# Performance work log

Measured on AMD Instinct MI355X. Metric: run time of the kernel, lower is better.

Reference implementation:

```python
import jax, jax.numpy as jnp
import numpy as np

B, S, D, H, E, K = 2, 2048, 1024, 2048, 8, 2


def setup_inputs() -> dict:
    key = jax.random.key(0)
    ks = jax.random.split(key, 9)
    sc_d = 1.0 / np.sqrt(D)
    sc_h = 1.0 / np.sqrt(H)
    return {
        "x": jax.random.normal(ks[0], (B, S, D), dtype=jnp.float32),
        "w_router": jax.random.normal(ks[1], (E, D), dtype=jnp.float32) * sc_d,
        "Wg": jax.random.normal(ks[2], (E, H, D), dtype=jnp.float32) * sc_d,  # per-expert gate proj (torch Linear weight layout [out,in])
        "Wu": jax.random.normal(ks[3], (E, H, D), dtype=jnp.float32) * sc_d,
        "Wd": jax.random.normal(ks[4], (E, D, H), dtype=jnp.float32) * sc_h,
        "sg": jax.random.normal(ks[5], (H, D), dtype=jnp.float32) * sc_d,  # shared expert
        "su": jax.random.normal(ks[6], (H, D), dtype=jnp.float32) * sc_d,
        "sd": jax.random.normal(ks[7], (D, H), dtype=jnp.float32) * sc_h,
    }


def reference(x, w_router, Wg, Wu, Wd, sg, su, sd):
    b, s, d = x.shape
    xf = x.reshape(-1, d)  # [T, D]

    # --- gating ---
    logits = jnp.einsum("td,ed->te", xf, w_router)
    probs = jax.nn.softmax(logits, axis=-1)  # [T, E]
    topw, topi = jax.lax.top_k(probs, K)  # [T, K]
    topw = topw / jnp.sum(topw, axis=-1, keepdims=True)
    # combine weights per (token, expert): topk indices are distinct per token
    comb = jnp.sum(topw[..., None] * jax.nn.one_hot(topi, E, dtype=xf.dtype), axis=1)  # [T, E]

    # --- shared expert (SwiGLU) ---
    shared = jnp.einsum(
        "th,dh->td",
        jax.nn.silu(jnp.einsum("td,hd->th", xf, sg)) * jnp.einsum("td,hd->th", xf, su),
        sd,
    )

    # --- routed experts: dense all-expert compute, weighted combine ---
    h1 = jax.nn.silu(jnp.einsum("td,ehd->teh", xf, Wg))
    h2 = jnp.einsum("td,ehd->teh", xf, Wu)
    eo = jnp.einsum("teh,edh->ted", h1 * h2, Wd)  # [T, E, D]
    routed = jnp.einsum("te,ted->td", comb, eo)

    return (routed + shared).reshape(b, s, d)
```

## Files before the change

### kernel.cpp

```cpp
#include <hip/hip_runtime.h>
#include <hip/hip_bf16.h>

#define T_TOK 4096
#define D_DIM 1024
#define H_DIM 2048

typedef __attribute__((ext_vector_type(8))) short short8;
typedef __attribute__((ext_vector_type(4))) float floatx4;

__device__ __forceinline__ unsigned short f2bf(float f) {
  unsigned int u = __builtin_bit_cast(unsigned int, f);
  return (unsigned short)((u + 0x7fffu + ((u >> 16) & 1u)) >> 16);
}

__device__ __forceinline__ float bf2f(unsigned short s) {
  unsigned int u = ((unsigned int)s) << 16;
  return __builtin_bit_cast(float, u);
}

__device__ __forceinline__ void glds16(const ushort* g, ushort* l) {
  __builtin_amdgcn_global_load_lds(
      (const __attribute__((address_space(1))) unsigned int*)g,
      (__attribute__((address_space(3))) unsigned int*)l, 16, 0, 0);
}

__global__ void cvt_kernel(const float4* __restrict__ Wg, ushort4* __restrict__ Wgb,
                           const float4* __restrict__ Wu, ushort4* __restrict__ Wub,
                           const float4* __restrict__ sg, ushort4* __restrict__ sgb,
                           const float4* __restrict__ su, ushort4* __restrict__ sub) {
  int id = blockIdx.x * 256 + threadIdx.x;
  const float4* s; ushort4* d; int i;
  if (id < 4194304)      { s = Wg; d = Wgb; i = id; }
  else if (id < 8388608) { s = Wu; d = Wub; i = id - 4194304; }
  else if (id < 8912896) { s = sg; d = sgb; i = id - 8388608; }
  else                   { s = su; d = sub; i = id - 8912896; }
  float4 v = s[i];
  ushort4 o;
  o.x = f2bf(v.x); o.y = f2bf(v.y); o.z = f2bf(v.z); o.w = f2bf(v.w);
  d[i] = o;
}

__global__ void router_kernel(const float* __restrict__ x, const float* __restrict__ wr,
                              ushort* __restrict__ xb,
                              int* __restrict__ topi, float2* __restrict__ topw) {
  const int w = threadIdx.x >> 6;
  const int l = threadIdx.x & 63;
  const int t = blockIdx.x * 4 + w;
  const float4* xr = (const float4*)(x + (size_t)t * D_DIM);
  ushort4* xo = (ushort4*)(xb + (size_t)t * D_DIM);
  float p[8];
#pragma unroll
  for (int e = 0; e < 8; ++e) p[e] = 0.f;
#pragma unroll
  for (int i = 0; i < 4; ++i) {
    float4 xv = xr[i * 64 + l];
    ushort4 o;
    o.x = f2bf(xv.x); o.y = f2bf(xv.y); o.z = f2bf(xv.z); o.w = f2bf(xv.w);
    xo[i * 64 + l] = o;
#pragma unroll
    for (int e = 0; e < 8; ++e) {
      float4 wv = ((const float4*)(wr + e * D_DIM))[i * 64 + l];
      p[e] += xv.x * wv.x + xv.y * wv.y + xv.z * wv.z + xv.w * wv.w;
    }
  }
#pragma unroll
  for (int off = 32; off > 0; off >>= 1) {
#pragma unroll
    for (int e = 0; e < 8; ++e) p[e] += __shfl_xor(p[e], off, 64);
  }
  if (l == 0) {
    float mx = p[0];
#pragma unroll
    for (int e = 1; e < 8; ++e) mx = fmaxf(mx, p[e]);
    float pr[8];
#pragma unroll
    for (int e = 0; e < 8; ++e) pr[e] = __expf(p[e] - mx);
    int i0 = 0;
#pragma unroll
    for (int e = 1; e < 8; ++e) if (pr[e] > pr[i0]) i0 = e;
    int i1 = (i0 == 0) ? 1 : 0;
#pragma unroll
    for (int e = 0; e < 8; ++e) if (e != i0 && pr[e] > pr[i1]) i1 = e;
    float w0 = pr[i0], w1 = pr[i1];
    float inv = 1.f / (w0 + w1);
    topi[t] = i0 | (i1 << 8);
    topw[t] = make_float2(w0 * inv, w1 * inv);
  }
}

__global__ void build_lists_kernel(const int* __restrict__ topi,
                                   int* __restrict__ counts, int* __restrict__ list,
                                   int* __restrict__ pos) {
  const int e = blockIdx.x;
  const int tid = threadIdx.x;
  const int l = tid & 63;
  const int w = tid >> 6;
  __shared__ int wtot[4];
  int base = 0;
  for (int c = 0; c < T_TOK; c += 256) {
    int t = c + tid;
    int ti = topi[t];
    int e0 = ti & 255, e1 = ti >> 8;
    bool flag = (e0 == e) || (e1 == e);
    unsigned long long m = __ballot(flag);
    int lanepos = __popcll(m & ((1ull << l) - 1ull));
    if (l == 0) wtot[w] = __popcll(m);
    __syncthreads();
    int waveoff = 0;
#pragma unroll
    for (int i = 0; i < 4; ++i) waveoff += (i < w) ? wtot[i] : 0;
    int tot = wtot[0] + wtot[1] + wtot[2] + wtot[3];
    if (flag) {
      int p = base + waveoff + lanepos;
      list[e * T_TOK + p] = t;
      int slot = (e0 == e) ? 0 : 1;
      pos[t * 2 + slot] = p;
    }
    base += tot;
    __syncthreads();
  }
  if (tid == 0) counts[e] = base;
}

__global__ __launch_bounds__(256, 2)
void gemm1_kernel(const ushort* __restrict__ xb,
                  const ushort* __restrict__ Wgb, const ushort* __restrict__ Wub,
                  const ushort* __restrict__ sgb, const ushort* __restrict__ sub,
                  const float4* __restrict__ Wd, ushort4* __restrict__ Wdb,
                  const float4* __restrict__ sd, ushort4* __restrict__ sdb,
                  const int* __restrict__ list, const int* __restrict__ counts,
                  ushort* __restrict__ h) {
  const int tid = threadIdx.x;
  {
    int bid = blockIdx.x + 16 * blockIdx.y + 512 * blockIdx.z;
#pragma unroll
    for (int it = 0; it < 4; ++it) {
      int idx = (bid * 4 + it) * 256 + tid;
      if (idx < 4194304) {
        float4 v = Wd[idx];
        ushort4 o;
        o.x = f2bf(v.x); o.y = f2bf(v.y); o.z = f2bf(v.z); o.w = f2bf(v.w);
        Wdb[idx] = o;
      }
    }
    if (bid < 2048) {
      int idx = bid * 256 + tid;
      float4 v = sd[idx];
      ushort4 o;
      o.x = f2bf(v.x); o.y = f2bf(v.y); o.z = f2bf(v.z); o.w = f2bf(v.w);
      sdb[idx] = o;
    }
  }

  const int e = blockIdx.z;
  int n_e, hbase;
  {
    int acc = 0, ce = 0;
    for (int q = 0; q < 8; ++q) {
      int c = counts[q];
      if (q < e) acc += c;
      if (q == e) ce = c;
    }
    n_e = (e == 8) ? T_TOK : ce;
    hbase = (e == 8) ? 8192 : acc;
  }
  const int r0 = blockIdx.y * 128;
  if (r0 >= n_e) return;
  const int c0 = blockIdx.x * 128;
  const ushort* Wg = (e == 8) ? sgb : (Wgb + (size_t)e * H_DIM * D_DIM);
  const ushort* Wu = (e == 8) ? sub : (Wub + (size_t)e * H_DIM * D_DIM);
  const int hrow0 = hbase + r0;

  __shared__ __align__(16) ushort As[128 * 64];
  __shared__ __align__(16) ushort Bgs[128 * 64];
  __shared__ __align__(16) ushort Bus[128 * 64];
  __shared__ int toks[128];

  const int l = tid & 63;
  const int w = tid >> 6;

  if (tid < 128) {
    int rr = r0 + tid;
    toks[tid] = (e == 8) ? ((rr < T_TOK) ? rr : (T_TOK - 1))
                         : list[e * T_TOK + ((rr < n_e) ? rr : (n_e - 1))];
  }
  __syncthreads();

  const int lrow8 = l >> 3;
  const int csw = (((l & 7) ^ lrow8) << 3);
  const ushort* ap[4];
#pragma unroll
  for (int i = 0; i < 4; ++i) {
    int ri = (w * 4 + i) * 8 + lrow8;
    ap[i] = xb + (size_t)toks[ri] * D_DIM + csw;
  }
  const ushort* bgp = Wg + (size_t)(c0 + w * 32 + lrow8) * D_DIM + csw;
  const ushort* bup = Wu + (size_t)(c0 + w * 32 + lrow8) * D_DIM + csw;

  floatx4 accg[4][4], accu[4][4];
#pragma unroll
  for (int i = 0; i < 4; ++i)
#pragma unroll
    for (int j = 0; j < 4; ++j) {
      accg[i][j] = (floatx4)(0.f);
      accu[i][j] = (floatx4)(0.f);
    }

  const int mrow = (w & 1) * 64;
  const int ncol = (w >> 1) * 64;
  int rba[4], rbb[4];
#pragma unroll
  for (int i = 0; i < 4; ++i) {
    rba[i] = (mrow + 16 * i + (l & 15)) * 64;
    rbb[i] = (ncol + 16 * i + (l & 15)) * 64;
  }

  for (int k0 = 0; k0 < D_DIM; k0 += 64) {
    __syncthreads();
#pragma unroll
    for (int i = 0; i < 4; ++i) {
      glds16(ap[i] + k0,                As  + (w * 4 + i) * 512);
      glds16(bgp + k0 + i * 8 * D_DIM,  Bgs + (w * 4 + i) * 512);
      glds16(bup + k0 + i * 8 * D_DIM,  Bus + (w * 4 + i) * 512);
    }
    __syncthreads();
#pragma unroll
    for (int s = 0; s < 2; ++s) {
      const int pq = ((((s << 2) | (l >> 4)) ^ (l & 7)) << 3);
      short8 a[4], bg[4], bu[4];
#pragma unroll
      for (int i = 0; i < 4; ++i) a[i] = *(const short8*)(As + rba[i] + pq);
#pragma unroll
      for (int j = 0; j < 4; ++j) {
        bg[j] = *(const short8*)(Bgs + rbb[j] + pq);
        bu[j] = *(const short8*)(Bus + rbb[j] + pq);
      }
#pragma unroll
      for (int i = 0; i < 4; ++i)
#pragma unroll
        for (int j = 0; j < 4; ++j) {
          accg[i][j] = __builtin_amdgcn_mfma_f32_16x16x32_bf16(a[i], bg[j], accg[i][j], 0, 0, 0);
          accu[i][j] = __builtin_amdgcn_mfma_f32_16x16x32_bf16(a[i], bu[j], accu[i][j], 0, 0, 0);
        }
    }
  }

#pragma unroll
  for (int i = 0; i < 4; ++i) {
#pragma unroll
    for (int r = 0; r < 4; ++r) {
      int lrow = mrow + 16 * i + (l >> 4) * 4 + r;
      if (r0 + lrow < n_e) {
#pragma unroll
        for (int j = 0; j < 4; ++j) {
          float g = accg[i][j][r];
          float u = accu[i][j][r];
          float hv = (g / (1.f + __expf(-g))) * u;
          int col = c0 + ncol + 16 * j + (l & 15);
          h[(size_t)(hrow0 + lrow) * H_DIM + col] = f2bf(hv);
        }
      }
    }
  }
}

__global__ __launch_bounds__(256, 3)
void gemm2_kernel(const ushort* __restrict__ h,
                  const ushort* __restrict__ Wdb, const ushort* __restrict__ sdb,
                  const int* __restrict__ counts,
                  ushort* __restrict__ eo) {
  const int e = blockIdx.z;
  int n_e, hbase;
  {
    int acc = 0, ce = 0;
    for (int q = 0; q < 8; ++q) {
      int c = counts[q];
      if (q < e) acc += c;
      if (q == e) ce = c;
    }
    n_e = (e == 8) ? T_TOK : ce;
    hbase = (e == 8) ? 8192 : acc;
  }
  const int r0 = blockIdx.y * 128;
  if (r0 >= n_e) return;
  const int c0 = blockIdx.x * 128;
  const ushort* Wd = (e == 8) ? sdb : (Wdb + (size_t)e * D_DIM * H_DIM);
  const int hrow0 = hbase + r0;

  __shared__ __align__(16) ushort As[128 * 64];
  __shared__ __align__(16) ushort Bs[128 * 64];

  const int tid = threadIdx.x;
  const int l = tid & 63;
  const int w = tid >> 6;

  const int lrow8 = l >> 3;
  const int csw = (((l & 7) ^ lrow8) << 3);
  const ushort* apb = h  + (size_t)(hrow0 + w * 32 + lrow8) * H_DIM + csw;
  const ushort* bpb = Wd + (size_t)(c0 + w * 32 + lrow8) * H_DIM + csw;

  floatx4 acc[4][4];
#pragma unroll
  for (int i = 0; i < 4; ++i)
#pragma unroll
    for (int j = 0; j < 4; ++j) acc[i][j] = (floatx4)(0.f);

  const int mrow = (w & 1) * 64;
  const int ncol = (w >> 1) * 64;
  int rba[4], rbb[4];
#pragma unroll
  for (int i = 0; i < 4; ++i) {
    rba[i] = (mrow + 16 * i + (l & 15)) * 64;
    rbb[i] = (ncol + 16 * i + (l & 15)) * 64;
  }

  for (int k0 = 0; k0 < H_DIM; k0 += 64) {
    __syncthreads();
#pragma unroll
    for (int i = 0; i < 4; ++i) {
      glds16(apb + k0 + i * 8 * H_DIM, As + (w * 4 + i) * 512);
      glds16(bpb + k0 + i * 8 * H_DIM, Bs + (w * 4 + i) * 512);
    }
    __syncthreads();
#pragma unroll
    for (int s = 0; s < 2; ++s) {
      const int pq = ((((s << 2) | (l >> 4)) ^ (l & 7)) << 3);
      short8 a[4], b[4];
#pragma unroll
      for (int i = 0; i < 4; ++i) a[i] = *(const short8*)(As + rba[i] + pq);
#pragma unroll
      for (int j = 0; j < 4; ++j) b[j] = *(const short8*)(Bs + rbb[j] + pq);
#pragma unroll
      for (int i = 0; i < 4; ++i)
#pragma unroll
        for (int j = 0; j < 4; ++j)
          acc[i][j] = __builtin_amdgcn_mfma_f32_16x16x32_bf16(a[i], b[j], acc[i][j], 0, 0, 0);
    }
  }

#pragma unroll
  for (int i = 0; i < 4; ++i) {
#pragma unroll
    for (int r = 0; r < 4; ++r) {
      int lrow = mrow + 16 * i + (l >> 4) * 4 + r;
      if (r0 + lrow < n_e) {
#pragma unroll
        for (int j = 0; j < 4; ++j) {
          int col = c0 + ncol + 16 * j + (l & 15);
          eo[(size_t)(hrow0 + lrow) * D_DIM + col] = f2bf(acc[i][j][r]);
        }
      }
    }
  }
}

__global__ void combine_kernel(const ushort* __restrict__ eo, const int* __restrict__ topi,
                               const float2* __restrict__ topw, const int* __restrict__ pos,
                               const int* __restrict__ counts, float* __restrict__ out) {
  const int t = blockIdx.x;
  const int c4 = threadIdx.x;
  int ti = topi[t];
  int e0 = ti & 255, e1 = ti >> 8;
  int off0 = 0, off1 = 0;
#pragma unroll
  for (int q = 0; q < 8; ++q) {
    int c = counts[q];
    off0 += (q < e0) ? c : 0;
    off1 += (q < e1) ? c : 0;
  }
  float2 wv = topw[t];
  int2 p = ((const int2*)pos)[t];
  const ushort4* ra = (const ushort4*)(eo + (size_t)(off0 + p.x) * D_DIM);
  const ushort4* rb = (const ushort4*)(eo + (size_t)(off1 + p.y) * D_DIM);
  const ushort4* rs = (const ushort4*)(eo + (size_t)(8192 + t) * D_DIM);
  ushort4 a = ra[c4], b = rb[c4], s = rs[c4];
  float4 o;
  o.x = wv.x * bf2f(a.x) + wv.y * bf2f(b.x) + bf2f(s.x);
  o.y = wv.x * bf2f(a.y) + wv.y * bf2f(b.y) + bf2f(s.y);
  o.z = wv.x * bf2f(a.z) + wv.y * bf2f(b.z) + bf2f(s.z);
  o.w = wv.x * bf2f(a.w) + wv.y * bf2f(b.w) + bf2f(s.w);
  ((float4*)(out + (size_t)t * D_DIM))[c4] = o;
}

#define OFF_XB   0ull
#define OFF_WGB  (OFF_XB + 8388608ull)
#define OFF_WUB  (OFF_WGB + 33554432ull)
#define OFF_WDB  (OFF_WUB + 33554432ull)
#define OFF_SGB  (OFF_WDB + 33554432ull)
#define OFF_SUB  (OFF_SGB + 4194304ull)
#define OFF_SDB  (OFF_SUB + 4194304ull)
#define OFF_H    (OFF_SDB + 4194304ull)
#define OFF_EO   OFF_WGB
#define OFF_CNT  (OFF_H + 50331648ull)
#define OFF_LIST (OFF_CNT + 64ull)
#define OFF_POS  (OFF_LIST + 131072ull)
#define OFF_TOPI (OFF_POS + 32768ull)
#define OFF_TOPW (OFF_TOPI + 16384ull)

extern "C" void kernel_launch(void* const* d_in, const int* in_sizes, int n_in,
                              void* d_out, int out_size, void* d_ws, size_t ws_size,
                              hipStream_t stream) {
  const float* x  = (const float*)d_in[0];
  const float* wr = (const float*)d_in[1];
  const float* Wg = (const float*)d_in[2];
  const float* Wu = (const float*)d_in[3];
  const float* Wd = (const float*)d_in[4];
  const float* sg = (const float*)d_in[5];
  const float* su = (const float*)d_in[6];
  const float* sd = (const float*)d_in[7];
  float* out = (float*)d_out;
  char* ws = (char*)d_ws;

  ushort* xb  = (ushort*)(ws + OFF_XB);
  ushort* Wgb = (ushort*)(ws + OFF_WGB);
  ushort* Wub = (ushort*)(ws + OFF_WUB);
  ushort* Wdb = (ushort*)(ws + OFF_WDB);
  ushort* sgb = (ushort*)(ws + OFF_SGB);
  ushort* sub = (ushort*)(ws + OFF_SUB);
  ushort* sdb = (ushort*)(ws + OFF_SDB);
  ushort* hbuf = (ushort*)(ws + OFF_H);
  ushort* eo   = (ushort*)(ws + OFF_EO);
  int* counts = (int*)(ws + OFF_CNT);
  int* list   = (int*)(ws + OFF_LIST);
  int* pos    = (int*)(ws + OFF_POS);
  int* topi   = (int*)(ws + OFF_TOPI);
  float2* topw = (float2*)(ws + OFF_TOPW);

  cvt_kernel<<<36864, 256, 0, stream>>>((const float4*)Wg, (ushort4*)Wgb,
                                        (const float4*)Wu, (ushort4*)Wub,
                                        (const float4*)sg, (ushort4*)sgb,
                                        (const float4*)su, (ushort4*)sub);

  router_kernel<<<1024, 256, 0, stream>>>(x, wr, xb, topi, topw);
  build_lists_kernel<<<8, 256, 0, stream>>>(topi, counts, list, pos);

  gemm1_kernel<<<dim3(16, 32, 9), 256, 0, stream>>>(xb, Wgb, Wub, sgb, sub,
                                                    (const float4*)Wd, (ushort4*)Wdb,
                                                    (const float4*)sd, (ushort4*)sdb,
                                                    list, counts, hbuf);
  gemm2_kernel<<<dim3(8, 32, 9), 256, 0, stream>>>(hbuf, Wdb, sdb, counts, eo);
  combine_kernel<<<4096, 256, 0, stream>>>(eo, topi, topw, pos, counts, out);
}
```

Baseline: 475.8 us.

## Merge weight conversion and router into one prep kernel; widen gemm2 N tile

The weight-to-bf16 conversion and the router kernel are merged into a single prep launch, and the Wd/sd conversion moves there out of gemm1's prologue. gemm2's output tile grows from 128x128 to 128x256, with 8 accumulator column blocks per wave and half as many blocks in x. The aim is to cut launch count, take conversion work off the GEMM's critical path, and raise A-tile reuse in gemm2. The cost is more registers per thread (occupancy hint lowered to 2), fewer gemm2 blocks, and serialising the Wd conversion before gemm1 where it used to overlap.

```diff
diff --git a/kernel.cpp b/kernel.cpp
--- a/kernel.cpp
+++ b/kernel.cpp
@@ -24,28 +24,33 @@
       (__attribute__((address_space(3))) unsigned int*)l, 16, 0, 0);
 }
 
-__global__ void cvt_kernel(const float4* __restrict__ Wg, ushort4* __restrict__ Wgb,
-                           const float4* __restrict__ Wu, ushort4* __restrict__ Wub,
-                           const float4* __restrict__ sg, ushort4* __restrict__ sgb,
-                           const float4* __restrict__ su, ushort4* __restrict__ sub) {
-  int id = blockIdx.x * 256 + threadIdx.x;
-  const float4* s; ushort4* d; int i;
-  if (id < 4194304)      { s = Wg; d = Wgb; i = id; }
-  else if (id < 8388608) { s = Wu; d = Wub; i = id - 4194304; }
-  else if (id < 8912896) { s = sg; d = sgb; i = id - 8388608; }
-  else                   { s = su; d = sub; i = id - 8912896; }
-  float4 v = s[i];
-  ushort4 o;
-  o.x = f2bf(v.x); o.y = f2bf(v.y); o.z = f2bf(v.z); o.w = f2bf(v.w);
-  d[i] = o;
-}
-
-__global__ void router_kernel(const float* __restrict__ x, const float* __restrict__ wr,
-                              ushort* __restrict__ xb,
-                              int* __restrict__ topi, float2* __restrict__ topw) {
+__global__ void prep_kernel(const float4* __restrict__ Wg, ushort4* __restrict__ Wgb,
+                            const float4* __restrict__ Wu, ushort4* __restrict__ Wub,
+                            const float4* __restrict__ Wd, ushort4* __restrict__ Wdb,
+                            const float4* __restrict__ sg, ushort4* __restrict__ sgb,
+                            const float4* __restrict__ su, ushort4* __restrict__ sub,
+                            const float4* __restrict__ sd, ushort4* __restrict__ sdb,
+                            const float* __restrict__ x, const float* __restrict__ wr,
+                            ushort* __restrict__ xb,
+                            int* __restrict__ topi, float2* __restrict__ topw) {
+  if (blockIdx.x < 55296) {
+    int id = blockIdx.x * 256 + threadIdx.x;
+    const float4* s; ushort4* d; int i;
+    if (id < 4194304)       { s = Wg; d = Wgb; i = id; }
+    else if (id < 8388608)  { s = Wu; d = Wub; i = id - 4194304; }
+    else if (id < 12582912) { s = Wd; d = Wdb; i = id - 8388608; }
+    else if (id < 13107200) { s = sg; d = sgb; i = id - 12582912; }
+    else if (id < 13631488) { s = su; d = sub; i = id - 13107200; }
+    else                    { s = sd; d = sdb; i = id - 13631488; }
+    float4 v = s[i];
+    ushort4 o;
+    o.x = f2bf(v.x); o.y = f2bf(v.y); o.z = f2bf(v.z); o.w = f2bf(v.w);
+    d[i] = o;
+    return;
+  }
   const int w = threadIdx.x >> 6;
   const int l = threadIdx.x & 63;
-  const int t = blockIdx.x * 4 + w;
+  const int t = (blockIdx.x - 55296) * 4 + w;
   const float4* xr = (const float4*)(x + (size_t)t * D_DIM);
   ushort4* xo = (ushort4*)(xb + (size_t)t * D_DIM);
   float p[8];
@@ -126,32 +131,8 @@
 void gemm1_kernel(const ushort* __restrict__ xb,
                   const ushort* __restrict__ Wgb, const ushort* __restrict__ Wub,
                   const ushort* __restrict__ sgb, const ushort* __restrict__ sub,
-                  const float4* __restrict__ Wd, ushort4* __restrict__ Wdb,
-                  const float4* __restrict__ sd, ushort4* __restrict__ sdb,
                   const int* __restrict__ list, const int* __restrict__ counts,
                   ushort* __restrict__ h) {
-  const int tid = threadIdx.x;
-  {
-    int bid = blockIdx.x + 16 * blockIdx.y + 512 * blockIdx.z;
-#pragma unroll
-    for (int it = 0; it < 4; ++it) {
-      int idx = (bid * 4 + it) * 256 + tid;
-      if (idx < 4194304) {
-        float4 v = Wd[idx];
-        ushort4 o;
-        o.x = f2bf(v.x); o.y = f2bf(v.y); o.z = f2bf(v.z); o.w = f2bf(v.w);
-        Wdb[idx] = o;
-      }
-    }
-    if (bid < 2048) {
-      int idx = bid * 256 + tid;
-      float4 v = sd[idx];
-      ushort4 o;
-      o.x = f2bf(v.x); o.y = f2bf(v.y); o.z = f2bf(v.z); o.w = f2bf(v.w);
-      sdb[idx] = o;
-    }
-  }
-
   const int e = blockIdx.z;
   int n_e, hbase;
   {
@@ -176,6 +157,7 @@
   __shared__ __align__(16) ushort Bus[128 * 64];
   __shared__ int toks[128];
 
+  const int tid = threadIdx.x;
   const int l = tid & 63;
   const int w = tid >> 6;
 
@@ -264,7 +246,7 @@
   }
 }
 
-__global__ __launch_bounds__(256, 3)
+__global__ __launch_bounds__(256, 2)
 void gemm2_kernel(const ushort* __restrict__ h,
                   const ushort* __restrict__ Wdb, const ushort* __restrict__ sdb,
                   const int* __restrict__ counts,
@@ -283,12 +265,12 @@
   }
   const int r0 = blockIdx.y * 128;
   if (r0 >= n_e) return;
-  const int c0 = blockIdx.x * 128;
+  const int c0 = blockIdx.x * 256;
   const ushort* Wd = (e == 8) ? sdb : (Wdb + (size_t)e * D_DIM * H_DIM);
   const int hrow0 = hbase + r0;
 
   __shared__ __align__(16) ushort As[128 * 64];
-  __shared__ __align__(16) ushort Bs[128 * 64];
+  __shared__ __align__(16) ushort Bs[256 * 64];
 
   const int tid = threadIdx.x;
   const int l = tid & 63;
@@ -297,43 +279,43 @@
   const int lrow8 = l >> 3;
   const int csw = (((l & 7) ^ lrow8) << 3);
   const ushort* apb = h  + (size_t)(hrow0 + w * 32 + lrow8) * H_DIM + csw;
-  const ushort* bpb = Wd + (size_t)(c0 + w * 32 + lrow8) * H_DIM + csw;
-
-  floatx4 acc[4][4];
+  const ushort* bpb = Wd + (size_t)(c0 + w * 64 + lrow8) * H_DIM + csw;
+
+  floatx4 acc[4][8];
 #pragma unroll
   for (int i = 0; i < 4; ++i)
 #pragma unroll
-    for (int j = 0; j < 4; ++j) acc[i][j] = (floatx4)(0.f);
+    for (int j = 0; j < 8; ++j) acc[i][j] = (floatx4)(0.f);
 
   const int mrow = (w & 1) * 64;
-  const int ncol = (w >> 1) * 64;
-  int rba[4], rbb[4];
-#pragma unroll
-  for (int i = 0; i < 4; ++i) {
-    rba[i] = (mrow + 16 * i + (l & 15)) * 64;
-    rbb[i] = (ncol + 16 * i + (l & 15)) * 64;
-  }
+  const int ncol = (w >> 1) * 128;
+  int rba[4], rbb[8];
+#pragma unroll
+  for (int i = 0; i < 4; ++i) rba[i] = (mrow + 16 * i + (l & 15)) * 64;
+#pragma unroll
+  for (int j = 0; j < 8; ++j) rbb[j] = (ncol + 16 * j + (l & 15)) * 64;
 
   for (int k0 = 0; k0 < H_DIM; k0 += 64) {
     __syncthreads();
 #pragma unroll
-    for (int i = 0; i < 4; ++i) {
+    for (int i = 0; i < 4; ++i)
       glds16(apb + k0 + i * 8 * H_DIM, As + (w * 4 + i) * 512);
-      glds16(bpb + k0 + i * 8 * H_DIM, Bs + (w * 4 + i) * 512);
-    }
+#pragma unroll
+    for (int i = 0; i < 8; ++i)
+      glds16(bpb + k0 + i * 8 * H_DIM, Bs + (w * 8 + i) * 512);
     __syncthreads();
 #pragma unroll
     for (int s = 0; s < 2; ++s) {
       const int pq = ((((s << 2) | (l >> 4)) ^ (l & 7)) << 3);
-      short8 a[4], b[4];
+      short8 a[4], b[8];
 #pragma unroll
       for (int i = 0; i < 4; ++i) a[i] = *(const short8*)(As + rba[i] + pq);
 #pragma unroll
-      for (int j = 0; j < 4; ++j) b[j] = *(const short8*)(Bs + rbb[j] + pq);
+      for (int j = 0; j < 8; ++j) b[j] = *(const short8*)(Bs + rbb[j] + pq);
 #pragma unroll
       for (int i = 0; i < 4; ++i)
 #pragma unroll
-        for (int j = 0; j < 4; ++j)
+        for (int j = 0; j < 8; ++j)
           acc[i][j] = __builtin_amdgcn_mfma_f32_16x16x32_bf16(a[i], b[j], acc[i][j], 0, 0, 0);
     }
   }
@@ -345,7 +327,7 @@
       int lrow = mrow + 16 * i + (l >> 4) * 4 + r;
       if (r0 + lrow < n_e) {
 #pragma unroll
-        for (int j = 0; j < 4; ++j) {
+        for (int j = 0; j < 8; ++j) {
           int col = c0 + ncol + 16 * j + (l & 15);
           eo[(size_t)(hrow0 + lrow) * D_DIM + col] = f2bf(acc[i][j][r]);
         }
@@ -426,18 +408,17 @@
   int* topi   = (int*)(ws + OFF_TOPI);
   float2* topw = (float2*)(ws + OFF_TOPW);
 
-  cvt_kernel<<<36864, 256, 0, stream>>>((const float4*)Wg, (ushort4*)Wgb,
-                                        (const float4*)Wu, (ushort4*)Wub,
-                                        (const float4*)sg, (ushort4*)sgb,
-                                        (const float4*)su, (ushort4*)sub);
-
-  router_kernel<<<1024, 256, 0, stream>>>(x, wr, xb, topi, topw);
+  prep_kernel<<<56320, 256, 0, stream>>>((const float4*)Wg, (ushort4*)Wgb,
+                                         (const float4*)Wu, (ushort4*)Wub,
+                                         (const float4*)Wd, (ushort4*)Wdb,
+                                         (const float4*)sg, (ushort4*)sgb,
+                                         (const float4*)su, (ushort4*)sub,
+                                         (const float4*)sd, (ushort4*)sdb,
+                                         x, wr, xb, topi, topw);
   build_lists_kernel<<<8, 256, 0, stream>>>(topi, counts, list, pos);
 
   gemm1_kernel<<<dim3(16, 32, 9), 256, 0, stream>>>(xb, Wgb, Wub, sgb, sub,
-                                                    (const float4*)Wd, (ushort4*)Wdb,
-                                                    (const float4*)sd, (ushort4*)sdb,
                                                     list, counts, hbuf);
-  gemm2_kernel<<<dim3(8, 32, 9), 256, 0, stream>>>(hbuf, Wdb, sdb, counts, eo);
+  gemm2_kernel<<<dim3(4, 32, 9), 256, 0, stream>>>(hbuf, Wdb, sdb, counts, eo);
   combine_kernel<<<4096, 256, 0, stream>>>(eo, topi, topw, pos, counts, out);
 }
```

Result: faster. 447.2 us (-6.0%).
